# Kernel optimization log

Hardware: AMD Instinct MI355X
Metric: run time of the kernel (lower is better)

## Reference

```python
import jax, jax.numpy as jnp
import numpy as np

B, S_IN, S_CTX = 2, 4096, 512
INPUT_DIM = CTX_DIM = DIM = 1024
NUM_HEADS = 16
HEAD_DIM = DIM // NUM_HEADS
BASE = 10000.0


def rms_norm(x, scale, eps=1e-6):
    xf = x.astype(jnp.float32)
    rrms = jax.lax.rsqrt(jnp.mean(xf * xf, axis=-1, keepdims=True) + eps)
    return (xf * rrms).astype(x.dtype) * scale


def apply_rope(x, pos):
    # x: [B, N, H, D]; rotate-half RoPE over full head_dim
    d = x.shape[-1]
    inv_freq = 1.0 / (BASE ** (jnp.arange(0, d, 2, dtype=jnp.float32) / d))  # [d/2]
    ang = pos.astype(jnp.float32)[:, None] * inv_freq[None, :]  # [N, d/2]
    cos = jnp.cos(ang)[None, :, None, :]
    sin = jnp.sin(ang)[None, :, None, :]
    x1, x2 = x[..., : d // 2], x[..., d // 2 :]
    return jnp.concatenate([x1 * cos - x2 * sin, x2 * cos + x1 * sin], axis=-1).astype(x.dtype)


def setup_inputs() -> dict:
    key = jax.random.key(0)
    ks = jax.random.split(key, 8)
    std = 0.02
    return {
        "input": jax.random.normal(ks[0], (B, S_IN, INPUT_DIM), jnp.float32),
        "context": jax.random.normal(ks[1], (B, S_CTX, CTX_DIM), jnp.float32),
        "W_qkv_in": jax.random.normal(ks[2], (3 * DIM, INPUT_DIM), jnp.float32) * std,
        "b_qkv_in": jnp.zeros((3 * DIM,), jnp.float32),
        "W_qkv_ctx": jax.random.normal(ks[3], (3 * DIM, CTX_DIM), jnp.float32) * std,
        "b_qkv_ctx": jnp.zeros((3 * DIM,), jnp.float32),
        "q_scale_in": jnp.ones((DIM,), jnp.float32),
        "k_scale_in": jnp.ones((DIM,), jnp.float32),
        "q_scale_ctx": jnp.ones((DIM,), jnp.float32),
        "k_scale_ctx": jnp.ones((DIM,), jnp.float32),
        "W_out_in": jax.random.normal(ks[4], (INPUT_DIM, DIM), jnp.float32) * std,
        "b_out_in": jnp.zeros((INPUT_DIM,), jnp.float32),
        "W_out_ctx": jax.random.normal(ks[5], (CTX_DIM, DIM), jnp.float32) * std,
        "b_out_ctx": jnp.zeros((CTX_DIM,), jnp.float32),
    }


def reference(input, context, W_qkv_in, b_qkv_in, W_qkv_ctx, b_qkv_ctx,
              q_scale_in, k_scale_in, q_scale_ctx, k_scale_ctx,
              W_out_in, b_out_in, W_out_ctx, b_out_ctx):
    # dual-stream QKV projections
    qkv_i = input @ W_qkv_in.T + b_qkv_in        # [B, S_in, 3*DIM]
    qkv_c = context @ W_qkv_ctx.T + b_qkv_ctx    # [B, S_ctx, 3*DIM]
    qi, ki, vi = jnp.split(qkv_i, 3, axis=-1)
    qc, kc, vc = jnp.split(qkv_c, 3, axis=-1)
    # QK-RMSNorm over full dim (as in QKNorm(dim))
    qi, ki = rms_norm(qi, q_scale_in), rms_norm(ki, k_scale_in)
    qc, kc = rms_norm(qc, q_scale_ctx), rms_norm(kc, k_scale_ctx)
    # concat context first, then input
    q = jnp.concatenate([qc, qi], axis=1)  # [B, N, DIM]
    k = jnp.concatenate([kc, ki], axis=1)
    v = jnp.concatenate([vc, vi], axis=1)
    N = q.shape[1]
    pos = jnp.arange(N)
    # RoPE applied per head
    q = apply_rope(q.reshape(B, N, NUM_HEADS, HEAD_DIM), pos).reshape(B, N, DIM)
    k = apply_rope(k.reshape(B, N, NUM_HEADS, HEAD_DIM), pos).reshape(B, N, DIM)
    # single-head attention over full dim (faithful to source: heads flattened before q@k^T)
    scale = HEAD_DIM ** -0.5
    attn = jax.nn.softmax(jnp.einsum('bnd,bmd->bnm', q, k) * scale, axis=-1)
    out = jnp.einsum('bnm,bmd->bnd', attn, v)  # [B, N, DIM]
    s_ctx = context.shape[1]
    input_output = out[:, s_ctx:, :] @ W_out_in.T + b_out_in
    context_output = out[:, :s_ctx, :] @ W_out_ctx.T + b_out_ctx
    return (input_output, context_output)
```

## Files before the change

### kernel.cpp

```cpp
#include <hip/hip_runtime.h>
#include <stdint.h>

typedef unsigned short u16;
typedef __bf16 bf16x8 __attribute__((ext_vector_type(8)));
typedef float f32x4 __attribute__((ext_vector_type(4)));

typedef const __attribute__((address_space(1))) uint32_t* gu32p;
typedef __attribute__((address_space(3))) uint32_t* lu32p;
#define GLOAD_LDS16(g, l) \
  __builtin_amdgcn_global_load_lds((gu32p)(const void*)(g), (lu32p)(void*)(l), 16, 0, 0)

static __device__ __forceinline__ u16 f2bf(float f) {
  uint32_t u = __builtin_bit_cast(uint32_t, f);
  return (u16)((u + 0x7FFFu + ((u >> 16) & 1u)) >> 16);
}
static __device__ __forceinline__ float bf2f(u16 h) {
  uint32_t u = ((uint32_t)h) << 16;
  return __builtin_bit_cast(float, u);
}

__global__ __launch_bounds__(256) void k_f32_to_bf16(const float* __restrict__ in,
                                                     u16* __restrict__ out, int n) {
  int i = (blockIdx.x * 256 + threadIdx.x) * 4;
  if (i + 3 < n) {
    const float4 v = *(const float4*)&in[i];
    ushort4 o;
    o.x = f2bf(v.x); o.y = f2bf(v.y); o.z = f2bf(v.z); o.w = f2bf(v.w);
    *(ushort4*)&out[i] = o;
  }
}

__device__ __forceinline__ void gemm_bk64(const u16* __restrict__ A, const u16* __restrict__ Bt,
                                          int lda, int ldb, long row0, long col0,
                                          int kbeg, int kend, u16* smem, f32x4 acc[4][4]) {
  const int tid = threadIdx.x;
  const int l = tid & 63;
  const int w = tid >> 6;
  const int wm = w >> 1, wn = w & 1;
  const int lr = l & 15, kg = l >> 4;
  const int swz = (lr & 7) * 8;
  const int r_l = tid >> 3;
  const int ssrc = ((tid & 7) ^ (r_l & 7)) * 8;
  const u16* gA = &A[(row0 + r_l) * (long)lda + ssrc];
  const u16* gB = &Bt[(col0 + r_l) * (long)ldb + ssrc];
  u16* const ldsA = smem + w * 512;
  u16* const ldsB = smem + 8192 + w * 512;
  const int NT = (kend - kbeg) >> 6;

  {
#pragma unroll
    for (int c = 0; c < 4; ++c) {
      GLOAD_LDS16(gA + (c * 32) * (long)lda + kbeg, ldsA + c * 2048);
      GLOAD_LDS16(gB + (c * 32) * (long)ldb + kbeg, ldsB + c * 2048);
    }
  }
  asm volatile("s_waitcnt vmcnt(0)" ::: "memory");
  __builtin_amdgcn_s_barrier();
  __builtin_amdgcn_sched_barrier(0);

  for (int t = 0; t < NT; ++t) {
    const int d = (t & 1) << 14;
    const int dn = ((t + 1) & 1) << 14;
    const bool pf = (t + 1 < NT);
    const long k1 = kbeg + (long)(t + 1) * 64;
    bf16x8 af[4], bv[4];
    if (pf) {
#pragma unroll
      for (int c = 0; c < 4; ++c)
        GLOAD_LDS16(gA + (c * 32) * (long)lda + k1, ldsA + dn + c * 2048);
    }
#pragma unroll
    for (int i = 0; i < 4; ++i) {
      af[i] = *(const bf16x8*)&smem[d + (wm * 64 + i * 16 + lr) * 64 + (kg * 8 ^ swz)];
      bv[i] = *(const bf16x8*)&smem[d + 8192 + (wn * 64 + i * 16 + lr) * 64 + (kg * 8 ^ swz)];
    }
    __builtin_amdgcn_s_setprio(1);
#pragma unroll
    for (int mf = 0; mf < 4; ++mf)
#pragma unroll
      for (int nf = 0; nf < 4; ++nf)
        acc[mf][nf] = __builtin_amdgcn_mfma_f32_16x16x32_bf16(af[mf], bv[nf], acc[mf][nf], 0, 0, 0);
    __builtin_amdgcn_s_setprio(0);
    if (pf) {
#pragma unroll
      for (int c = 0; c < 4; ++c)
        GLOAD_LDS16(gB + (c * 32) * (long)ldb + k1, ldsB + dn + c * 2048);
    }
#pragma unroll
    for (int i = 0; i < 4; ++i) {
      af[i] = *(const bf16x8*)&smem[d + (wm * 64 + i * 16 + lr) * 64 + ((32 + kg * 8) ^ swz)];
      bv[i] = *(const bf16x8*)&smem[d + 8192 + (wn * 64 + i * 16 + lr) * 64 + ((32 + kg * 8) ^ swz)];
    }
    __builtin_amdgcn_s_setprio(1);
#pragma unroll
    for (int mf = 0; mf < 4; ++mf)
#pragma unroll
      for (int nf = 0; nf < 4; ++nf)
        acc[mf][nf] = __builtin_amdgcn_mfma_f32_16x16x32_bf16(af[mf], bv[nf], acc[mf][nf], 0, 0, 0);
    __builtin_amdgcn_s_setprio(0);
    asm volatile("s_waitcnt vmcnt(0)" ::: "memory");
    __builtin_amdgcn_s_barrier();
    __builtin_amdgcn_sched_barrier(0);
  }
}

#define EPI_VARS                                   \
  const int l = threadIdx.x & 63;                  \
  const int w = threadIdx.x >> 6;                  \
  const int wm = w >> 1, wn = w & 1;               \
  const int mrow = (l >> 4) * 4, ncol = l & 15;

__global__ __launch_bounds__(256, 2) void k_gemm_qkv(
    const u16* __restrict__ XIN, const u16* __restrict__ XCTX,
    const u16* __restrict__ WQI, const u16* __restrict__ WQC,
    const float* __restrict__ bqi, const float* __restrict__ bqc,
    u16* __restrict__ qb, u16* __restrict__ kb, u16* __restrict__ vt) {
  __shared__ u16 smem[32768];
  f32x4 acc[4][4] = {};
  const bool isCtx = blockIdx.x >= 64;
  const u16* X = isCtx ? XCTX : XIN;
  const u16* W = isCtx ? WQC : WQI;
  const float* bias = isCtx ? bqc : bqi;
  const int seg_start = isCtx ? 0 : 512;
  long row0 = (long)(isCtx ? blockIdx.x - 64 : blockIdx.x) * 128;
  long col0 = (long)blockIdx.y * 128;
  gemm_bk64(X, W, 1024, 1024, row0, col0, 0, 1024, smem, acc);
  EPI_VARS
#pragma unroll
  for (int mf = 0; mf < 4; ++mf)
#pragma unroll
    for (int nf = 0; nf < 4; ++nf)
#pragma unroll
      for (int r = 0; r < 4; ++r) {
        int m = (int)row0 + wm * 64 + mf * 16 + mrow + r;
        int n = (int)col0 + wn * 64 + nf * 16 + ncol;
        float v = acc[mf][nf][r] + bias[n];
        int b, s;
        if (isCtx) { b = m >> 9; s = m & 511; } else { b = m >> 12; s = m & 4095; }
        long grow = (long)b * 4608 + seg_start + s;
        if (n < 1024)      qb[grow * 1024 + n] = f2bf(v);
        else if (n < 2048) kb[grow * 1024 + (n - 1024)] = f2bf(v);
        else               vt[((long)b * 1024 + (n - 2048)) * 4608 + seg_start + s] = f2bf(v);
      }
}

__global__ __launch_bounds__(256) void k_normrope(u16* __restrict__ qb, u16* __restrict__ kb,
                                                  const float* __restrict__ qsi, const float* __restrict__ ksi,
                                                  const float* __restrict__ qsc, const float* __restrict__ ksc) {
  __shared__ float sm[4];
  const int row = blockIdx.x;
  const int which = blockIdx.y;
  const int n = row % 4608;
  u16* buf = which ? kb : qb;
  const float* scale = which ? (n < 512 ? ksc : ksi) : (n < 512 ? qsc : qsi);
  u16* rp = buf + (long)row * 1024;
  const int t = threadIdx.x;
  float x[4];
  int idx[4];
  float ss = 0.f;
#pragma unroll
  for (int i = 0; i < 2; ++i) {
    int p = t + i * 256;
    int h = p >> 5, j = p & 31;
    int e1 = h * 64 + j;
    idx[2 * i] = e1; idx[2 * i + 1] = e1 + 32;
    float a = bf2f(rp[e1]), b = bf2f(rp[e1 + 32]);
    x[2 * i] = a; x[2 * i + 1] = b;
    ss += a * a + b * b;
  }
#pragma unroll
  for (int o = 32; o; o >>= 1) ss += __shfl_xor(ss, o, 64);
  if ((t & 63) == 0) sm[t >> 6] = ss;
  __syncthreads();
  ss = sm[0] + sm[1] + sm[2] + sm[3];
  const float rr = rsqrtf(ss * (1.0f / 1024.0f) + 1e-6f);
#pragma unroll
  for (int i = 0; i < 2; ++i) {
    int p = t + i * 256;
    int j = p & 31;
    float x1 = x[2 * i] * rr * scale[idx[2 * i]];
    float x2 = x[2 * i + 1] * rr * scale[idx[2 * i + 1]];
    float freq = exp2f((float)j * (-13.287712379549449f / 32.0f));
    float ang = (float)n * freq;
    float sn, cs;
    sincosf(ang, &sn, &cs);
    rp[idx[2 * i]]     = f2bf(x1 * cs - x2 * sn);
    rp[idx[2 * i + 1]] = f2bf(x2 * cs + x1 * sn);
  }
}

__global__ __launch_bounds__(256, 2) void k_gemm_s(const u16* __restrict__ Q, const u16* __restrict__ Kb,
                                                   float* __restrict__ S) {
  __shared__ u16 smem[32768];
  f32x4 acc[4][4] = {};
  long row0 = (long)blockIdx.x * 128;
  long col0 = (long)blockIdx.y * 128;
  gemm_bk64(Q, Kb, 1024, 1024, row0, col0, 0, 1024, smem, acc);
  EPI_VARS
#pragma unroll
  for (int mf = 0; mf < 4; ++mf)
#pragma unroll
    for (int nf = 0; nf < 4; ++nf)
#pragma unroll
      for (int r = 0; r < 4; ++r) {
        long m = row0 + wm * 64 + mf * 16 + mrow + r;
        long n = col0 + wn * 64 + nf * 16 + ncol;
        S[m * 4608 + n] = acc[mf][nf][r] * 0.125f;
      }
}

__global__ __launch_bounds__(256) void k_softmax(const float* __restrict__ S, u16* __restrict__ P) {
  __shared__ float sm[4];
  const long row = blockIdx.x;
  const float* sr = S + row * 4608;
  const int t = threadIdx.x;
  float v[18];
  float mx = -3.4e38f;
#pragma unroll
  for (int i = 0; i < 18; ++i) { v[i] = sr[i * 256 + t]; mx = fmaxf(mx, v[i]); }
#pragma unroll
  for (int o = 32; o; o >>= 1) mx = fmaxf(mx, __shfl_xor(mx, o, 64));
  if ((t & 63) == 0) sm[t >> 6] = mx;
  __syncthreads();
  mx = fmaxf(fmaxf(sm[0], sm[1]), fmaxf(sm[2], sm[3]));
  __syncthreads();
  float sum = 0.f;
#pragma unroll
  for (int i = 0; i < 18; ++i) { v[i] = __expf(v[i] - mx); sum += v[i]; }
#pragma unroll
  for (int o = 32; o; o >>= 1) sum += __shfl_xor(sum, o, 64);
  if ((t & 63) == 0) sm[t >> 6] = sum;
  __syncthreads();
  sum = sm[0] + sm[1] + sm[2] + sm[3];
  const float inv = 1.0f / sum;
  u16* pr = P + row * 4608;
#pragma unroll
  for (int i = 0; i < 18; ++i) pr[i * 256 + t] = f2bf(v[i] * inv);
}

__global__ __launch_bounds__(256, 2) void k_gemm_o(const u16* __restrict__ P, const u16* __restrict__ VT,
                                                   float* __restrict__ OP) {
  __shared__ u16 smem[32768];
  f32x4 acc[4][4] = {};
  long row0 = (long)blockIdx.x * 128;
  long col0 = (long)blockIdx.y * 128;
  const int kc = blockIdx.z;
  gemm_bk64(P, VT, 4608, 4608, row0, col0, kc * 1152, (kc + 1) * 1152, smem, acc);
  float* op = OP + (long)kc * 4608 * 1024;
  EPI_VARS
#pragma unroll
  for (int mf = 0; mf < 4; ++mf)
#pragma unroll
    for (int nf = 0; nf < 4; ++nf)
#pragma unroll
      for (int r = 0; r < 4; ++r) {
        long m = row0 + wm * 64 + mf * 16 + mrow + r;
        long n = col0 + wn * 64 + nf * 16 + ncol;
        op[m * 1024 + n] = acc[mf][nf][r];
      }
}

__global__ __launch_bounds__(256) void k_reduce4(const float* __restrict__ OP, u16* __restrict__ AO) {
  const long st = 4608L * 1024;
  long i = ((long)blockIdx.x * 256 + threadIdx.x) * 4;
  float4 a = *(const float4*)&OP[i];
  float4 b = *(const float4*)&OP[i + st];
  float4 c = *(const float4*)&OP[i + 2 * st];
  float4 d = *(const float4*)&OP[i + 3 * st];
  ushort4 o;
  o.x = f2bf(a.x + b.x + c.x + d.x);
  o.y = f2bf(a.y + b.y + c.y + d.y);
  o.z = f2bf(a.z + b.z + c.z + d.z);
  o.w = f2bf(a.w + b.w + c.w + d.w);
  *(ushort4*)&AO[i] = o;
}

__global__ __launch_bounds__(256, 2) void k_gemm_out2(const u16* __restrict__ AO,
                                                      const u16* __restrict__ WOI, const u16* __restrict__ WOC,
                                                      const float* __restrict__ boi, const float* __restrict__ boc,
                                                      float* __restrict__ out) {
  __shared__ u16 smem[32768];
  f32x4 acc[4][4] = {};
  long row0 = (long)blockIdx.x * 128;
  long col0 = (long)blockIdx.y * 128;
  int b = (int)(row0 / 4608);
  int s0 = (int)(row0 % 4608);
  const bool ctx = s0 < 512;
  const u16* W = ctx ? WOC : WOI;
  const float* bias = ctx ? boc : boi;
  float* ob = ctx ? out + 8388608 + ((long)b * 512 + s0) * 1024
                  : out + ((long)b * 4096 + (s0 - 512)) * 1024;
  gemm_bk64(AO, W, 1024, 1024, row0, col0, 0, 1024, smem, acc);
  EPI_VARS
#pragma unroll
  for (int mf = 0; mf < 4; ++mf)
#pragma unroll
    for (int nf = 0; nf < 4; ++nf)
#pragma unroll
      for (int r = 0; r < 4; ++r) {
        long m = wm * 64 + mf * 16 + mrow + r;
        long n = col0 + wn * 64 + nf * 16 + ncol;
        ob[m * 1024 + n] = acc[mf][nf][r] + bias[n];
      }
}

extern "C" void kernel_launch(void* const* d_in, const int* in_sizes, int n_in,
                              void* d_out, int out_size, void* d_ws, size_t ws_size,
                              hipStream_t stream) {
  const float* input   = (const float*)d_in[0];
  const float* context = (const float*)d_in[1];
  const float* Wqi     = (const float*)d_in[2];
  const float* bqi     = (const float*)d_in[3];
  const float* Wqc     = (const float*)d_in[4];
  const float* bqc     = (const float*)d_in[5];
  const float* qsi     = (const float*)d_in[6];
  const float* ksi     = (const float*)d_in[7];
  const float* qsc     = (const float*)d_in[8];
  const float* ksc     = (const float*)d_in[9];
  const float* Woi     = (const float*)d_in[10];
  const float* boi     = (const float*)d_in[11];
  const float* Woc     = (const float*)d_in[12];
  const float* boc     = (const float*)d_in[13];
  float* out = (float*)d_out;

  uint8_t* ws = (uint8_t*)d_ws;
  u16* XIN  = (u16*)(ws + 0);
  u16* XCTX = (u16*)(ws + 16777216);
  u16* WQI  = (u16*)(ws + 18874368);
  u16* WQC  = (u16*)(ws + 25165824);
  u16* WOI  = (u16*)(ws + 31457280);
  u16* WOC  = (u16*)(ws + 33554432);
  u16* QB   = (u16*)(ws + 35651584);
  u16* KB   = (u16*)(ws + 54525952);
  u16* VT   = (u16*)(ws + 73400320);
  u16* AO   = (u16*)(ws + 92274688);
  float* S32 = (float*)(ws + 111149056);
  u16* PB   = (u16*)(ws + 196083712);

  k_f32_to_bf16<<<dim3(8192), 256, 0, stream>>>(input, XIN, 2 * 4096 * 1024);
  k_f32_to_bf16<<<dim3(1024), 256, 0, stream>>>(context, XCTX, 2 * 512 * 1024);
  k_f32_to_bf16<<<dim3(3072), 256, 0, stream>>>(Wqi, WQI, 3072 * 1024);
  k_f32_to_bf16<<<dim3(3072), 256, 0, stream>>>(Wqc, WQC, 3072 * 1024);
  k_f32_to_bf16<<<dim3(1024), 256, 0, stream>>>(Woi, WOI, 1024 * 1024);
  k_f32_to_bf16<<<dim3(1024), 256, 0, stream>>>(Woc, WOC, 1024 * 1024);

  k_gemm_qkv<<<dim3(72, 24), 256, 0, stream>>>(XIN, XCTX, WQI, WQC, bqi, bqc, QB, KB, VT);

  k_normrope<<<dim3(9216, 2), 256, 0, stream>>>(QB, KB, qsi, ksi, qsc, ksc);

  for (int b = 0; b < 2; ++b) {
    const u16* Qb  = QB + (long)b * 4608 * 1024;
    const u16* Kbp = KB + (long)b * 4608 * 1024;
    const u16* VTb = VT + (long)b * 1024 * 4608;
    u16* AOb = AO + (long)b * 4608 * 1024;
    k_gemm_s<<<dim3(36, 36), 256, 0, stream>>>(Qb, Kbp, S32);
    k_softmax<<<dim3(4608), 256, 0, stream>>>(S32, PB);
    k_gemm_o<<<dim3(36, 8, 4), 256, 0, stream>>>(PB, VTb, (float*)S32);
    k_reduce4<<<dim3(4608), 256, 0, stream>>>((const float*)S32, AOb);
  }

  k_gemm_out2<<<dim3(72, 8), 256, 0, stream>>>(AO, WOI, WOC, boi, boc, out);
}
```

Baseline: 480.7 us.

## Fuse input conversions, add XCD-aware block swizzle, vectorize norm-rope loads

Merges the six fp32-to-bf16 conversion launches into one kernel that picks its source by block index, removing launch overhead. Adds an XCD swizzle to all GEMM grids so that consecutive logical tiles are placed on the same XCD, aiming to improve L2 reuse of shared A/B panels. Rewrites norm+rope so each thread handles two adjacent elements with 32-bit loads and stores instead of scattered 16-bit accesses. The swizzle assumes the block count is divisible by 8, which holds for all of these grids.

```diff
diff --git a/kernel.cpp b/kernel.cpp
--- a/kernel.cpp
+++ b/kernel.cpp
@@ -19,15 +19,31 @@
   return __builtin_bit_cast(float, u);
 }
 
-__global__ __launch_bounds__(256) void k_f32_to_bf16(const float* __restrict__ in,
-                                                     u16* __restrict__ out, int n) {
-  int i = (blockIdx.x * 256 + threadIdx.x) * 4;
-  if (i + 3 < n) {
-    const float4 v = *(const float4*)&in[i];
-    ushort4 o;
-    o.x = f2bf(v.x); o.y = f2bf(v.y); o.z = f2bf(v.z); o.w = f2bf(v.w);
-    *(ushort4*)&out[i] = o;
-  }
+static __device__ __forceinline__ int xcd_swz(int bid, int nwg) {
+  const int c = nwg >> 3;
+  return (bid & 7) * c + (bid >> 3);
+}
+
+__global__ __launch_bounds__(256) void k_conv_all(
+    const float* __restrict__ s0, u16* __restrict__ d0,
+    const float* __restrict__ s1, u16* __restrict__ d1,
+    const float* __restrict__ s2, u16* __restrict__ d2,
+    const float* __restrict__ s3, u16* __restrict__ d3,
+    const float* __restrict__ s4, u16* __restrict__ d4,
+    const float* __restrict__ s5, u16* __restrict__ d5) {
+  int b = blockIdx.x;
+  const float* src; u16* dst; long off;
+  if (b < 8192)       { src = s0; dst = d0; off = (long)b * 1024; }
+  else if (b < 9216)  { src = s1; dst = d1; off = (long)(b - 8192) * 1024; }
+  else if (b < 12288) { src = s2; dst = d2; off = (long)(b - 9216) * 1024; }
+  else if (b < 15360) { src = s3; dst = d3; off = (long)(b - 12288) * 1024; }
+  else if (b < 16384) { src = s4; dst = d4; off = (long)(b - 15360) * 1024; }
+  else                { src = s5; dst = d5; off = (long)(b - 16384) * 1024; }
+  long i = off + threadIdx.x * 4;
+  const float4 v = *(const float4*)&src[i];
+  ushort4 o;
+  o.x = f2bf(v.x); o.y = f2bf(v.y); o.z = f2bf(v.z); o.w = f2bf(v.w);
+  *(ushort4*)&dst[i] = o;
 }
 
 __device__ __forceinline__ void gemm_bk64(const u16* __restrict__ A, const u16* __restrict__ Bt,
@@ -117,13 +133,15 @@
     u16* __restrict__ qb, u16* __restrict__ kb, u16* __restrict__ vt) {
   __shared__ u16 smem[32768];
   f32x4 acc[4][4] = {};
-  const bool isCtx = blockIdx.x >= 64;
+  const int f = xcd_swz(blockIdx.x + 72 * blockIdx.y, 72 * 24);
+  const int bx = f % 72, by = f / 72;
+  const bool isCtx = bx >= 64;
   const u16* X = isCtx ? XCTX : XIN;
   const u16* W = isCtx ? WQC : WQI;
   const float* bias = isCtx ? bqc : bqi;
   const int seg_start = isCtx ? 0 : 512;
-  long row0 = (long)(isCtx ? blockIdx.x - 64 : blockIdx.x) * 128;
-  long col0 = (long)blockIdx.y * 128;
+  long row0 = (long)(isCtx ? bx - 64 : bx) * 128;
+  long col0 = (long)by * 128;
   gemm_bk64(X, W, 1024, 1024, row0, col0, 0, 1024, smem, acc);
   EPI_VARS
 #pragma unroll
@@ -155,46 +173,41 @@
   const float* scale = which ? (n < 512 ? ksc : ksi) : (n < 512 ? qsc : qsi);
   u16* rp = buf + (long)row * 1024;
   const int t = threadIdx.x;
-  float x[4];
-  int idx[4];
-  float ss = 0.f;
-#pragma unroll
-  for (int i = 0; i < 2; ++i) {
-    int p = t + i * 256;
-    int h = p >> 5, j = p & 31;
-    int e1 = h * 64 + j;
-    idx[2 * i] = e1; idx[2 * i + 1] = e1 + 32;
-    float a = bf2f(rp[e1]), b = bf2f(rp[e1 + 32]);
-    x[2 * i] = a; x[2 * i + 1] = b;
-    ss += a * a + b * b;
-  }
+  const int h = t >> 4;
+  const int jj = (t & 15) * 2;
+  const int e1 = h * 64 + jj;
+  const int e2 = e1 + 32;
+  uint32_t u1 = *(const uint32_t*)&rp[e1];
+  uint32_t u2 = *(const uint32_t*)&rp[e2];
+  float x1a = bf2f((u16)u1), x1b = bf2f((u16)(u1 >> 16));
+  float x2a = bf2f((u16)u2), x2b = bf2f((u16)(u2 >> 16));
+  float ss = x1a * x1a + x1b * x1b + x2a * x2a + x2b * x2b;
 #pragma unroll
   for (int o = 32; o; o >>= 1) ss += __shfl_xor(ss, o, 64);
   if ((t & 63) == 0) sm[t >> 6] = ss;
   __syncthreads();
   ss = sm[0] + sm[1] + sm[2] + sm[3];
   const float rr = rsqrtf(ss * (1.0f / 1024.0f) + 1e-6f);
-#pragma unroll
-  for (int i = 0; i < 2; ++i) {
-    int p = t + i * 256;
-    int j = p & 31;
-    float x1 = x[2 * i] * rr * scale[idx[2 * i]];
-    float x2 = x[2 * i + 1] * rr * scale[idx[2 * i + 1]];
-    float freq = exp2f((float)j * (-13.287712379549449f / 32.0f));
-    float ang = (float)n * freq;
-    float sn, cs;
-    sincosf(ang, &sn, &cs);
-    rp[idx[2 * i]]     = f2bf(x1 * cs - x2 * sn);
-    rp[idx[2 * i + 1]] = f2bf(x2 * cs + x1 * sn);
-  }
+  float s1a = scale[e1], s1b = scale[e1 + 1], s2a = scale[e2], s2b = scale[e2 + 1];
+  x1a *= rr * s1a; x1b *= rr * s1b; x2a *= rr * s2a; x2b *= rr * s2b;
+  const float c = -13.287712379549449f / 32.0f;
+  float fa = exp2f((float)jj * c), fb = exp2f((float)(jj + 1) * c);
+  float sna, csa, snb, csb;
+  sincosf((float)n * fa, &sna, &csa);
+  sincosf((float)n * fb, &snb, &csb);
+  u16 o1a = f2bf(x1a * csa - x2a * sna), o1b = f2bf(x1b * csb - x2b * snb);
+  u16 o2a = f2bf(x2a * csa + x1a * sna), o2b = f2bf(x2b * csb + x1b * snb);
+  *(uint32_t*)&rp[e1] = (uint32_t)o1a | ((uint32_t)o1b << 16);
+  *(uint32_t*)&rp[e2] = (uint32_t)o2a | ((uint32_t)o2b << 16);
 }
 
 __global__ __launch_bounds__(256, 2) void k_gemm_s(const u16* __restrict__ Q, const u16* __restrict__ Kb,
                                                    float* __restrict__ S) {
   __shared__ u16 smem[32768];
   f32x4 acc[4][4] = {};
-  long row0 = (long)blockIdx.x * 128;
-  long col0 = (long)blockIdx.y * 128;
+  const int f = xcd_swz(blockIdx.x + 36 * blockIdx.y, 36 * 36);
+  long row0 = (long)(f % 36) * 128;
+  long col0 = (long)(f / 36) * 128;
   gemm_bk64(Q, Kb, 1024, 1024, row0, col0, 0, 1024, smem, acc);
   EPI_VARS
 #pragma unroll
@@ -242,8 +255,9 @@
                                                    float* __restrict__ OP) {
   __shared__ u16 smem[32768];
   f32x4 acc[4][4] = {};
-  long row0 = (long)blockIdx.x * 128;
-  long col0 = (long)blockIdx.y * 128;
+  const int f = xcd_swz(blockIdx.x + 36 * blockIdx.y, 36 * 8);
+  long row0 = (long)(f % 36) * 128;
+  long col0 = (long)(f / 36) * 128;
   const int kc = blockIdx.z;
   gemm_bk64(P, VT, 4608, 4608, row0, col0, kc * 1152, (kc + 1) * 1152, smem, acc);
   float* op = OP + (long)kc * 4608 * 1024;
@@ -281,8 +295,9 @@
                                                       float* __restrict__ out) {
   __shared__ u16 smem[32768];
   f32x4 acc[4][4] = {};
-  long row0 = (long)blockIdx.x * 128;
-  long col0 = (long)blockIdx.y * 128;
+  const int f = xcd_swz(blockIdx.x + 72 * blockIdx.y, 72 * 8);
+  long row0 = (long)(f % 72) * 128;
+  long col0 = (long)(f / 72) * 128;
   int b = (int)(row0 / 4608);
   int s0 = (int)(row0 % 4608);
   const bool ctx = s0 < 512;
@@ -337,12 +352,8 @@
   float* S32 = (float*)(ws + 111149056);
   u16* PB   = (u16*)(ws + 196083712);
 
-  k_f32_to_bf16<<<dim3(8192), 256, 0, stream>>>(input, XIN, 2 * 4096 * 1024);
-  k_f32_to_bf16<<<dim3(1024), 256, 0, stream>>>(context, XCTX, 2 * 512 * 1024);
-  k_f32_to_bf16<<<dim3(3072), 256, 0, stream>>>(Wqi, WQI, 3072 * 1024);
-  k_f32_to_bf16<<<dim3(3072), 256, 0, stream>>>(Wqc, WQC, 3072 * 1024);
-  k_f32_to_bf16<<<dim3(1024), 256, 0, stream>>>(Woi, WOI, 1024 * 1024);
-  k_f32_to_bf16<<<dim3(1024), 256, 0, stream>>>(Woc, WOC, 1024 * 1024);
+  k_conv_all<<<dim3(17408), 256, 0, stream>>>(input, XIN, context, XCTX, Wqi, WQI,
+                                              Wqc, WQC, Woi, WOI, Woc, WOC);
 
   k_gemm_qkv<<<dim3(72, 24), 256, 0, stream>>>(XIN, XCTX, WQI, WQC, bqi, bqc, QB, KB, VT);
 
```

Result: slower. 536.8 us (+11.7%).
